# Performance work log

Measured on AMD Instinct MI355X. Metric: run time of the kernel, lower is better.

Reference implementation:

```python
import jax, jax.numpy as jnp
import numpy as np

N_HEAD = 16
N_EMBD = 1024
B, T = 4, 1024


def setup_inputs() -> dict:
    key = jax.random.key(0)
    ks = jax.random.split(key, 8)
    hs = N_EMBD // N_HEAD
    x = jax.random.normal(ks[0], (B, T, N_EMBD), dtype=jnp.float32)
    # previous-layer attention load per token, ~O(1/T) like a softmax column mean
    refractory_state = jax.random.uniform(ks[1], (B, T), dtype=jnp.float32) / T
    s_attn = 1.0 / np.sqrt(N_EMBD)
    W_attn = jax.random.normal(ks[2], (N_EMBD, 3 * N_EMBD), dtype=jnp.float32) * s_attn
    b_attn = jnp.zeros((3 * N_EMBD,), dtype=jnp.float32)
    W_proj = jax.random.normal(ks[3], (N_EMBD, N_EMBD), dtype=jnp.float32) * s_attn
    b_proj = jnp.zeros((N_EMBD,), dtype=jnp.float32)
    # learnable LIF params, init per module (lif_mode='refractory')
    threshold = jnp.full((N_HEAD,), 0.01, dtype=jnp.float32)
    leak = jnp.full((N_HEAD,), 2.0, dtype=jnp.float32)
    steepness = jnp.full((N_HEAD,), 2.0, dtype=jnp.float32)
    ref_strength = jnp.full((N_HEAD,), -2.0, dtype=jnp.float32)
    cross_w = jnp.full((N_HEAD,), -2.0, dtype=jnp.float32)
    return {
        "x": x, "refractory_state": refractory_state,
        "W_attn": W_attn, "b_attn": b_attn,
        "W_proj": W_proj, "b_proj": b_proj,
        "threshold": threshold, "leak": leak, "steepness": steepness,
        "ref_strength": ref_strength, "cross_w": cross_w,
    }


def reference(x, refractory_state, W_attn, b_attn, W_proj, b_proj,
              threshold, leak, steepness, ref_strength, cross_w):
    Bq, Tq, C = x.shape
    H = N_HEAD
    hs = C // H
    qkv = x @ W_attn + b_attn                     # [B,T,3C]
    q, k, v = jnp.split(qkv, 3, axis=-1)
    q = q.reshape(Bq, Tq, H, hs).transpose(0, 2, 1, 3)  # [B,H,T,hs]
    k = k.reshape(Bq, Tq, H, hs).transpose(0, 2, 1, 3)
    v = v.reshape(Bq, Tq, H, hs).transpose(0, 2, 1, 3)

    att = jnp.einsum('bhqd,bhkd->bhqk', q, k) * (1.0 / jnp.sqrt(jnp.asarray(hs, x.dtype)))
    causal = jnp.tril(jnp.ones((Tq, Tq), dtype=bool))
    att = jnp.where(causal[None, None], att, -jnp.inf)
    probs = jax.nn.softmax(att, axis=-1)          # [B,H,T,T]

    thr = (jnp.abs(threshold) * 0.1)[None, :, None, None]
    lk = jax.nn.sigmoid(leak)[None, :, None, None]
    st = jax.nn.softplus(steepness)[None, :, None, None]
    # refractory: column load over queries + cross-layer load
    column_load = probs.mean(axis=-2, keepdims=True)          # [B,H,1,T]
    eff_thr = thr + jax.nn.softplus(ref_strength)[None, :, None, None] * column_load
    eff_thr = eff_thr + jax.nn.sigmoid(cross_w)[None, :, None, None] * refractory_state[:, None, None, :]

    fire = jax.nn.sigmoid(st * (probs - eff_thr))
    lif_w = fire + lk * (1.0 - fire)
    mod = probs * lif_w
    mod = mod / (mod.sum(axis=-1, keepdims=True) + 1e-8)
    new_refractory = mod.mean(axis=1).mean(axis=-2)           # [B,T]

    y = jnp.einsum('bhqk,bhkd->bhqd', mod, v)
    y = y.transpose(0, 2, 1, 3).reshape(Bq, Tq, C)
    y = y @ W_proj + b_proj
    return y, new_refractory
```

## Files before the change

kernel.cpp:

```cpp
#include <hip/hip_runtime.h>
#include <math.h>

#define B_  4
#define T_  1024
#define C_  1024
#define H_  16
#define HS_ 64
#define K2E 0.1803368801f
#define LOG2E 1.44269504f

typedef _Float16 f16;
typedef _Float16 f16x8 __attribute__((ext_vector_type(8)));
typedef _Float16 f16x4 __attribute__((ext_vector_type(4)));
typedef float f32x4 __attribute__((ext_vector_type(4)));

#define MFMA16(a,b,c) __builtin_amdgcn_mfma_f32_16x16x32_f16(a,b,c,0,0,0)
#define EXP2(x) __builtin_amdgcn_exp2f(x)
#define RCP(x)  __builtin_amdgcn_rcpf(x)

#define PSTRIDE_BH 557056

__device__ __forceinline__ float qsum_(float v){
    v += __shfl_xor(v,1,64); v += __shfl_xor(v,2,64);
    v += __shfl_xor(v,4,64); v += __shfl_xor(v,8,64);
    return v;
}
__device__ __forceinline__ float sigmoidf_(float x){ return 1.0f/(1.0f + __expf(-x)); }
__device__ __forceinline__ float softplusf_(float x){ return fmaxf(x, 0.0f) + log1pf(__expf(-fabsf(x))); }

__device__ __forceinline__ void gload_lds16(const f16* g, f16* l){
    __builtin_amdgcn_global_load_lds(
        (__attribute__((address_space(1))) void*)(void*)g,
        (__attribute__((address_space(3))) void*)(void*)l, 16, 0, 0);
}

__global__ __launch_bounds__(256) void prep_k(
    const float* __restrict__ x, const float* __restrict__ Wa,
    const float* __restrict__ Wp,
    f16* __restrict__ x_h, f16* __restrict__ WaT, f16* __restrict__ WpT,
    float* __restrict__ zbase)
{
    __shared__ float tl[32][33];
    const int bid = blockIdx.x, tid = threadIdx.x;
    if (bid < 2048){
        int i = bid*256 + tid;
        const float4* p = (const float4*)x + (size_t)i*2;
        float4 a = p[0], b = p[1];
        f16x8 o;
        o[0]=(f16)a.x; o[1]=(f16)a.y; o[2]=(f16)a.z; o[3]=(f16)a.w;
        o[4]=(f16)b.x; o[5]=(f16)b.y; o[6]=(f16)b.z; o[7]=(f16)b.w;
        *((f16x8*)x_h + i) = o;
    } else if (bid < 5120){
        int t = bid - 2048;
        int n0 = (t % 96)*32, k0 = (t / 96)*32;
        const int c = tid & 31, r4 = tid >> 5;
        #pragma unroll
        for (int i=0;i<4;i++){ int r = r4*4+i; tl[r][c] = Wa[(size_t)(k0+r)*3072 + n0 + c]; }
        __syncthreads();
        #pragma unroll
        for (int i=0;i<4;i++){ int r = r4*4+i; WaT[(size_t)(n0+r)*1024 + k0 + c] = (f16)tl[c][r]; }
    } else if (bid < 6144){
        int t = bid - 5120;
        int n0 = (t & 31)*32, k0 = (t >> 5)*32;
        const int c = tid & 31, r4 = tid >> 5;
        #pragma unroll
        for (int i=0;i<4;i++){ int r = r4*4+i; tl[r][c] = Wp[(size_t)(k0+r)*1024 + n0 + c]; }
        __syncthreads();
        #pragma unroll
        for (int i=0;i<4;i++){ int r = r4*4+i; WpT[(size_t)(n0+r)*1024 + k0 + c] = (f16)tl[c][r]; }
    } else {
        int idx = (bid - 6144)*256 + tid;
        float4 z; z.x=0.f; z.y=0.f; z.z=0.f; z.w=0.f;
        ((float4*)zbase)[idx] = z;
    }
}

#define CT_STRIDE 132
__global__ __launch_bounds__(256) void gemm_qkv_k(
    const f16* __restrict__ A, const f16* __restrict__ Bt,
    const float* __restrict__ bias,
    f16* __restrict__ Qh, f16* __restrict__ Kh, f16* __restrict__ Vt)
{
    __shared__ __align__(16) f16 smem[16896];
    const int tid = threadIdx.x;
    const int lane = tid & 63, wave = tid >> 6;
    const int lx = lane & 15, quad = lane >> 4;
    const int wm = wave & 1, wn = wave >> 1;
    const int lin = blockIdx.y*24 + blockIdx.x;
    const int nb  = (lin & 7)*96 + (lin >> 3);
    const int m0 = (nb/24)*128, n0 = (nb%24)*128;
    const f16* Ap = A  + (size_t)m0*1024;
    const f16* Bp = Bt + (size_t)n0*1024;
    f32x4 acc[4][4];
    #pragma unroll
    for (int i=0;i<4;i++){
        #pragma unroll
        for (int j=0;j<4;j++){ acc[i][j][0]=0.f;acc[i][j][1]=0.f;acc[i][j][2]=0.f;acc[i][j][3]=0.f; }
    }
#define GQ_STAGE(BUF, KT) { \
    const int k0s = (KT)*32; \
    for (int i=0;i<2;i++){ int c=i*4+wave; \
        gload_lds16(Ap + (size_t)(c*16+lx)*1024 + k0s + quad*8, &smem[(BUF) + c*512]); \
        gload_lds16(Bp + (size_t)(c*16+lx)*1024 + k0s + quad*8, &smem[(BUF) + 4096 + c*512]); } }
#define GQ_COMP(BUF) { \
    f16x8 af[4], bf[4]; \
    for (int mt=0;mt<4;mt++) af[mt] = *(const f16x8*)&smem[(BUF) + (wm*4+mt)*512 + quad*128 + lx*8]; \
    for (int nt=0;nt<4;nt++) bf[nt] = *(const f16x8*)&smem[(BUF) + 4096 + (wn*4+nt)*512 + quad*128 + lx*8]; \
    for (int mt=0;mt<4;mt++) \
        for (int nt=0;nt<4;nt++) \
            acc[mt][nt] = MFMA16(af[mt], bf[nt], acc[mt][nt]); }

    GQ_STAGE(0, 0);
    __syncthreads();
    #pragma unroll 1
    for (int it=0; it<32; it+=2){
        if (it+1 < 32) GQ_STAGE(8192, it+1);
        GQ_COMP(0);
        __syncthreads();
        if (it+2 < 32) GQ_STAGE(0, it+2);
        GQ_COMP(8192);
        __syncthreads();
    }
    f16* Ct = smem;
    #pragma unroll
    for (int mt=0;mt<4;mt++){
        #pragma unroll
        for (int nt=0;nt<4;nt++){
            int n_loc = wn*64 + nt*16 + lx;
            float bv = bias[n0 + n_loc];
            #pragma unroll
            for (int r=0;r<4;r++){
                int m_loc = wm*64 + mt*16 + quad*4 + r;
                Ct[m_loc*CT_STRIDE + n_loc] = (f16)(acc[mt][nt][r] + bv);
            }
        }
    }
    __syncthreads();
    const int bb = m0 >> 10;
    if (n0 < 2048){
        for (int it=0; it<8; it++){
            int row = it*32 + wave*8 + (lane>>3);
            int ch  = lane & 7;
            int m_loc = row >> 1, half = row & 1;
            f16x8 v = *(const f16x8*)&Ct[m_loc*CT_STRIDE + half*64 + ch*8];
            int n = n0 + half*64;
            int which = n >> 10, cc = n & 1023, h = cc >> 6;
            int t = (m0 + m_loc) & 1023;
            f16* dst = (which==0) ? Qh : Kh;
            *(f16x8*)(dst + ((size_t)(bb*16+h)*1024 + t)*64 + ch*8) = v;
        }
    } else {
        for (int it=0; it<8; it++){
            int drow = it*16 + wave*4 + (lane>>4);
            int ch   = lane & 15;
            int cc = (n0 + drow) & 1023;
            int h = cc >> 6, d = cc & 63;
            f16 tmp[8];
            #pragma unroll
            for (int j=0;j<8;j++) tmp[j] = Ct[(ch*8+j)*CT_STRIDE + drow];
            int t = (m0 + ch*8) & 1023;
            *(f16x8*)(Vt + ((size_t)(bb*16+h)*64 + d)*1024 + t) = *(f16x8*)tmp;
        }
    }
}

__global__ __launch_bounds__(256) void gemm_proj_k(
    const f16* __restrict__ A, const f16* __restrict__ Bt,
    const float* __restrict__ bias, float* __restrict__ out,
    const float* __restrict__ racc)
{
    if (blockIdx.x == 512){
        float* oref = out + (size_t)B_*T_*C_;
        #pragma unroll
        for (int j=0;j<16;j++){
            int idx = j*256 + threadIdx.x;
            oref[idx] = racc[idx] * (1.0f/(H_*T_));
        }
        return;
    }
    __shared__ __align__(16) f16 smem[12288];
    const int tid = threadIdx.x;
    const int lane = tid & 63, wave = tid >> 6;
    const int lx = lane & 15, quad = lane >> 4;
    const int wm = wave & 1, wn = wave >> 1;
    const int lin = blockIdx.x;
    const int nb  = (lin & 7)*64 + (lin >> 3);
    const int m0 = (nb >> 4)*128, n0 = (nb & 15)*64;
    const f16* Ap = A  + (size_t)m0*1024;
    const f16* Bp = Bt + (size_t)n0*1024;
    f32x4 acc[4][2];
    #pragma unroll
    for (int i=0;i<4;i++){
        #pragma unroll
        for (int j=0;j<2;j++){ acc[i][j][0]=0.f;acc[i][j][1]=0.f;acc[i][j][2]=0.f;acc[i][j][3]=0.f; }
    }
#define GP_STAGE(BUF, KT) { \
    const int k0s = (KT)*32; \
    for (int i=0;i<2;i++){ int c=i*4+wave; \
        gload_lds16(Ap + (size_t)(c*16+lx)*1024 + k0s + quad*8, &smem[(BUF) + c*512]); } \
    gload_lds16(Bp + (size_t)(wave*16+lx)*1024 + k0s + quad*8, &smem[(BUF) + 4096 + wave*512]); }
#define GP_COMP(BUF) { \
    f16x8 af[4], bf[2]; \
    for (int mt=0;mt<4;mt++) af[mt] = *(const f16x8*)&smem[(BUF) + (wm*4+mt)*512 + quad*128 + lx*8]; \
    for (int nt=0;nt<2;nt++) bf[nt] = *(const f16x8*)&smem[(BUF) + 4096 + (wn*2+nt)*512 + quad*128 + lx*8]; \
    for (int mt=0;mt<4;mt++) \
        for (int nt=0;nt<2;nt++) \
            acc[mt][nt] = MFMA16(af[mt], bf[nt], acc[mt][nt]); }

    GP_STAGE(0, 0);
    __syncthreads();
    #pragma unroll 1
    for (int it=0; it<32; it+=2){
        if (it+1 < 32) GP_STAGE(6144, it+1);
        GP_COMP(0);
        __syncthreads();
        if (it+2 < 32) GP_STAGE(0, it+2);
        GP_COMP(6144);
        __syncthreads();
    }
    #pragma unroll
    for (int mt=0;mt<4;mt++){
        #pragma unroll
        for (int nt=0;nt<2;nt++){
            int n = n0 + wn*32 + nt*16 + lx;
            float bv = bias[n];
            #pragma unroll
            for (int r=0;r<4;r++){
                int m = m0 + wm*64 + mt*16 + quad*4 + r;
                out[(size_t)m*1024 + n] = acc[mt][nt][r] + bv;
            }
        }
    }
}

__global__ __launch_bounds__(256) void attn_stats_k(
    const f16* __restrict__ Qh, const f16* __restrict__ Kh,
    float* __restrict__ rowl, float* __restrict__ colp,
    f16* __restrict__ Pbuf)
{
    __shared__ __align__(16) f16 Pl[4][16*72];
    __shared__ float invl_sh[64];
    const int tid = threadIdx.x;
    const int lane = tid & 63, wave = tid >> 6;
    const int lx = lane & 15, quad = lane >> 4;
    const int g  = 15 - (blockIdx.x >> 6);
    const int bh = blockIdx.x & 63;
    const int qpos = wave*16 + quad*4;
    const size_t kbase = (size_t)bh*65536;
    const int S = (g+1)*64;
    f16* __restrict__ Pblk = Pbuf + (size_t)bh*PSTRIDE_BH + (size_t)4096*((g*(g+1))>>1);

    const size_t qoff = ((size_t)bh*1024 + g*64 + wave*16 + lx)*64;
    f16x8 aq0 = *(const f16x8*)(Qh + qoff + quad*8);
    f16x8 aq1 = *(const f16x8*)(Qh + qoff + 32 + quad*8);

#define KLOADX(dst, KT) { \
    for (int nt=0;nt<4;nt++){ \
        const f16* kp = Kh + kbase + (size_t)((KT)*64 + nt*16 + lx)*64 + quad*8; \
        dst[nt*2]   = *(const f16x8*)(kp); \
        dst[nt*2+1] = *(const f16x8*)(kp + 32); } }
#define STATS_TILE(KT, rk) { \
    const bool diag = ((KT) == g); \
    for (int nt=0;nt<4;nt++){ \
        f32x4 sc = {0.f,0.f,0.f,0.f}; \
        sc = MFMA16(aq0, rk[nt*2],   sc); \
        sc = MFMA16(aq1, rk[nt*2+1], sc); \
        for (int r=0;r<4;r++){ \
            float sv = sc[r]; \
            if (diag && (nt*16+lx) > (qpos + r)) sv = -1e4f; \
            float p = EXP2(sv*K2E); \
            ls[r] += p; \
            Pl[wave][(quad*4+r)*72 + nt*16 + lx] = (f16)p; \
        } } \
    for (int it2=0; it2<2; it2++){ \
        int qq = it2*8 + (lane>>3), chh = lane & 7; \
        f16x8 v = *(const f16x8*)&Pl[wave][qq*72 + chh*8]; \
        *(f16x8*)(Pblk + (size_t)(wave*16+qq)*S + (KT)*64 + chh*8) = v; } }

    f16x8 rkE[8], rkO[8];
    float ls[4] = {0.f,0.f,0.f,0.f};
    KLOADX(rkE, 0);
    if (g >= 1) KLOADX(rkO, 1);
    #pragma unroll 1
    for (int kt=0; kt<=g; kt+=2){
        STATS_TILE(kt, rkE);
        if (kt+2 <= g) KLOADX(rkE, kt+2);
        if (kt+1 <= g){
            STATS_TILE(kt+1, rkO);
            if (kt+3 <= g) KLOADX(rkO, kt+3);
        }
    }
    #pragma unroll
    for (int r=0;r<4;r++){
        float l = qsum_(ls[r]);
        if (lx == 0){
            rowl[(size_t)bh*1024 + g*64 + qpos + r] = l;
            invl_sh[qpos + r] = RCP(l);
        }
    }
    __syncthreads();
    if (tid < (g+1)*16){
        const int k0 = tid*4;
        float a0=0.f, a1=0.f, a2=0.f, a3=0.f;
        const f16* pr = Pblk + k0;
        #pragma unroll 4
        for (int q=0;q<64;q++){
            f16x4 v = *(const f16x4*)(pr + (size_t)q*S);
            float w = invl_sh[q];
            a0 += (float)v[0]*w; a1 += (float)v[1]*w;
            a2 += (float)v[2]*w; a3 += (float)v[3]*w;
        }
        float* cp = colp + (size_t)bh*1024 + k0;
        atomicAdd(cp+0,a0); atomicAdd(cp+1,a1);
        atomicAdd(cp+2,a2); atomicAdd(cp+3,a3);
    }
}

__global__ __launch_bounds__(256) void attn_apply_k(
    const f16* __restrict__ Vt,
    const float* __restrict__ rowl,
    const float* __restrict__ colp, const float* __restrict__ refr,
    const float* __restrict__ threshold, const float* __restrict__ leak,
    const float* __restrict__ steepness, const float* __restrict__ ref_strength,
    const float* __restrict__ cross_w,
    f16* __restrict__ Yh, float* __restrict__ racc,
    f16* __restrict__ Pbuf)
{
    __shared__ __align__(16) f16 Pl[4][16*72];
    __shared__ float eb[1024];
    __shared__ float invl_sh[64];
    __shared__ float invD_sh[64];
    const int tid = threadIdx.x;
    const int lane = tid & 63, wave = tid >> 6;
    const int lx = lane & 15, quad = lane >> 4;
    const int g  = 15 - (blockIdx.x >> 6);
    const int bh = blockIdx.x & 63;
    const int b  = bh >> 4, h = bh & 15;
    const size_t kbase = (size_t)bh*65536;
    const int S = (g+1)*64;
    f16* __restrict__ Pblk = Pbuf + (size_t)bh*PSTRIDE_BH + (size_t)4096*((g*(g+1))>>1);

    const float thr = fabsf(threshold[h])*0.1f;
    const float lk  = sigmoidf_(leak[h]);
    const float st2 = softplusf_(steepness[h]) * LOG2E;
    const float sprT= softplusf_(ref_strength[h]) * (1.0f/T_);
    const float cw  = sigmoidf_(cross_w[h]);
    const float Alk = 1.f - lk;

    {
        float4 cp = *(const float4*)(colp + (size_t)bh*1024 + tid*4);
        float4 rf = *(const float4*)(refr + (size_t)b*1024 + tid*4);
        eb[tid*4+0] = st2*(thr + sprT*cp.x + cw*rf.x);
        eb[tid*4+1] = st2*(thr + sprT*cp.y + cw*rf.y);
        eb[tid*4+2] = st2*(thr + sprT*cp.z + cw*rf.z);
        eb[tid*4+3] = st2*(thr + sprT*cp.w + cw*rf.w);
    }
    if (tid < 64) invl_sh[tid] = RCP(rowl[(size_t)bh*1024 + g*64 + tid]);
    __syncthreads();

    const float wli = invl_sh[wave*16 + lx];

    f32x4 y[4];
    #pragma unroll
    for (int i=0;i<4;i++){ y[i][0]=0.f;y[i][1]=0.f;y[i][2]=0.f;y[i][3]=0.f; }
    float Dp = 0.f;

#define PLOADX(dst, KT) { \
    const f16* pp = Pblk + (size_t)(wave*16 + lx)*S + (KT)*64 + quad*8; \
    dst[0] = *(const f16x8*)(pp); \
    dst[1] = *(const f16x8*)(pp + 32); }
#define RVLOAD(dst, KT) { \
    for (int dt=0;dt<4;dt++){ \
        const f16* vp = Vt + kbase + (size_t)(dt*16 + lx)*1024 + (KT)*64 + quad*8; \
        dst[dt*2]   = *(const f16x8*)(vp); \
        dst[dt*2+1] = *(const f16x8*)(vp + 32); } }
#define LIF_TILE(KT, pv, af0, af1) { \
    const float* ebp = &eb[(KT)*64 + quad*8]; \
    float4 eA0 = *(const float4*)(ebp); \
    float4 eA1 = *(const float4*)(ebp+4); \
    float4 eB0 = *(const float4*)(ebp+32); \
    float4 eB1 = *(const float4*)(ebp+36); \
    float ea[8] = {eA0.x,eA0.y,eA0.z,eA0.w,eA1.x,eA1.y,eA1.z,eA1.w}; \
    float ebb[8] = {eB0.x,eB0.y,eB0.z,eB0.w,eB1.x,eB1.y,eB1.z,eB1.w}; \
    for (int jj=0;jj<8;jj++){ \
        float p = (float)pv[0][jj] * wli; \
        float fire = RCP(1.f + EXP2(ea[jj] - st2*p)); \
        float pw = p*(lk + Alk*fire); \
        Dp += pw; af0[jj] = (f16)pw; } \
    for (int jj=0;jj<8;jj++){ \
        float p = (float)pv[1][jj] * wli; \
        float fire = RCP(1.f + EXP2(ebb[jj] - st2*p)); \
        float pw = p*(lk + Alk*fire); \
        Dp += pw; af1[jj] = (f16)pw; } }
#define MFMA8(af0, af1, rv) { \
    for (int dt=0;dt<4;dt++){ \
        y[dt] = MFMA16(af0, rv[dt*2],   y[dt]); \
        y[dt] = MFMA16(af1, rv[dt*2+1], y[dt]); } }

    f16x8 rv[8], pvE[2], pvO[2], af0, af1;
    PLOADX(pvE, 0);
    if (g >= 1) PLOADX(pvO, 1);
    #pragma unroll 1
    for (int kt=0; kt<=g; kt+=2){
        RVLOAD(rv, kt);
        LIF_TILE(kt, pvE, af0, af1);
        if (kt+2 <= g) PLOADX(pvE, kt+2);
        MFMA8(af0, af1, rv);
        if (kt+1 <= g){
            RVLOAD(rv, kt+1);
            LIF_TILE(kt+1, pvO, af0, af1);
            if (kt+3 <= g) PLOADX(pvO, kt+3);
            MFMA8(af0, af1, rv);
        }
    }
    Dp += __shfl_xor(Dp,16,64); Dp += __shfl_xor(Dp,32,64);
    float invDl = RCP(Dp + 1e-8f);
    if (quad == 0) invD_sh[wave*16 + lx] = invDl;

    float invD[4];
    #pragma unroll
    for (int r=0;r<4;r++) invD[r] = invD_sh[wave*16 + quad*4 + r];
    #pragma unroll
    for (int dt=0;dt<4;dt++){
        #pragma unroll
        for (int r=0;r<4;r++)
            Pl[wave][(quad*4+r)*72 + dt*16 + lx] = (f16)(y[dt][r]*invD[r]);
    }
    #pragma unroll
    for (int it=0; it<2; it++){
        int q = it*8 + (lane>>3), ch = lane & 7;
        f16x8 v = *(const f16x8*)&Pl[wave][q*72 + ch*8];
        *(f16x8*)(Yh + (size_t)(b*1024 + g*64 + wave*16 + q)*1024 + h*64 + ch*8) = v;
    }

    __syncthreads();

    if (tid < (g+1)*16){
        const int k0 = tid*4;
        float4 ebv = *(const float4*)&eb[k0];
        float a0=0.f, a1=0.f, a2=0.f, a3=0.f;
        const f16* pr = Pblk + k0;
        #pragma unroll 4
        for (int q=0;q<64;q++){
            f16x4 v = *(const f16x4*)(pr + (size_t)q*S);
            float wl = invl_sh[q], wd = invD_sh[q];
            float p0 = (float)v[0]*wl, p1 = (float)v[1]*wl;
            float p2 = (float)v[2]*wl, p3 = (float)v[3]*wl;
            float f0 = RCP(1.f + EXP2(ebv.x - st2*p0));
            float f1 = RCP(1.f + EXP2(ebv.y - st2*p1));
            float f2 = RCP(1.f + EXP2(ebv.z - st2*p2));
            float f3 = RCP(1.f + EXP2(ebv.w - st2*p3));
            a0 += p0*(lk + Alk*f0)*wd; a1 += p1*(lk + Alk*f1)*wd;
            a2 += p2*(lk + Alk*f2)*wd; a3 += p3*(lk + Alk*f3)*wd;
        }
        float* rp = racc + (size_t)b*1024 + k0;
        atomicAdd(rp+0,a0); atomicAdd(rp+1,a1);
        atomicAdd(rp+2,a2); atomicAdd(rp+3,a3);
    }
}

extern "C" void kernel_launch(void* const* d_in, const int* in_sizes, int n_in,
                              void* d_out, int out_size, void* d_ws, size_t ws_size,
                              hipStream_t stream) {
    (void)in_sizes; (void)n_in; (void)out_size; (void)ws_size;
    const float* x           = (const float*)d_in[0];
    const float* refr        = (const float*)d_in[1];
    const float* W_attn      = (const float*)d_in[2];
    const float* b_attn      = (const float*)d_in[3];
    const float* W_proj      = (const float*)d_in[4];
    const float* b_proj      = (const float*)d_in[5];
    const float* threshold   = (const float*)d_in[6];
    const float* leak        = (const float*)d_in[7];
    const float* steepness   = (const float*)d_in[8];
    const float* ref_strength= (const float*)d_in[9];
    const float* cross_w     = (const float*)d_in[10];
    float* out = (float*)d_out;

    char* ws = (char*)d_ws;
    f16* x_h = (f16*)ws;                       ws += (size_t)4096*1024*2;
    f16* WaT = (f16*)ws;                       ws += (size_t)3072*1024*2;
    f16* WpT = (f16*)ws;                       ws += (size_t)1024*1024*2;
    f16* Qh  = (f16*)ws;                       ws += (size_t)64*1024*64*2;
    f16* Kh  = (f16*)ws;                       ws += (size_t)64*1024*64*2;
    f16* Vt  = (f16*)ws;                       ws += (size_t)64*64*1024*2;
    f16* Yh  = (f16*)ws;                       ws += (size_t)4096*1024*2;
    float* rowl = (float*)ws;                  ws += (size_t)65536*4;
    float* colp = (float*)ws;                  ws += (size_t)65536*4;
    float* racc = (float*)ws;                  ws += (size_t)4096*4;
    f16* Pbuf = (f16*)ws;                      ws += (size_t)64*PSTRIDE_BH*2;

    prep_k<<<dim3(6212), dim3(256), 0, stream>>>(x, W_attn, W_proj, x_h, WaT, WpT, colp);
    gemm_qkv_k<<<dim3(24,32), dim3(256), 0, stream>>>(x_h, WaT, b_attn, Qh, Kh, Vt);
    attn_stats_k<<<dim3(1024), dim3(256), 0, stream>>>(Qh, Kh, rowl, colp, Pbuf);
    attn_apply_k<<<dim3(1024), dim3(256), 0, stream>>>(
        Vt, rowl, colp, refr,
        threshold, leak, steepness, ref_strength, cross_w, Yh, racc, Pbuf);
    gemm_proj_k<<<dim3(513), dim3(256), 0, stream>>>(Yh, WpT, b_proj, out, racc);
}
```

Measured before the change: 293.0 us.

## Stage K tiles through shared memory and double-buffer V loads in LIF pass

In the stats kernel, each wave now loads a quarter of each K tile into registers and writes it into a double-buffered LDS tile. All four waves then read the full tile from LDS, so the same K rows are no longer fetched from global memory by every wave. This cuts K register footprint from 16 to 4 vectors but adds block barriers per tile. In the LIF/PV kernel, V tiles are prefetched into two register sets one tile ahead, and MFMA blocks are raised in wave priority with s_setprio. This increases register pressure.

```diff
diff --git a/kernel.cpp b/kernel.cpp
--- a/kernel.cpp
+++ b/kernel.cpp
@@ -238,6 +238,7 @@
     float* __restrict__ rowl, float* __restrict__ colp,
     f16* __restrict__ Pbuf)
 {
+    __shared__ __align__(16) f16 Kl[8192];
     __shared__ __align__(16) f16 Pl[4][16*72];
     __shared__ float invl_sh[64];
     const int tid = threadIdx.x;
@@ -254,17 +255,20 @@
     f16x8 aq0 = *(const f16x8*)(Qh + qoff + quad*8);
     f16x8 aq1 = *(const f16x8*)(Qh + qoff + 32 + quad*8);
 
-#define KLOADX(dst, KT) { \
-    for (int nt=0;nt<4;nt++){ \
-        const f16* kp = Kh + kbase + (size_t)((KT)*64 + nt*16 + lx)*64 + quad*8; \
-        dst[nt*2]   = *(const f16x8*)(kp); \
-        dst[nt*2+1] = *(const f16x8*)(kp + 32); } }
-#define STATS_TILE(KT, rk) { \
+#define KLOAD(dst, KT) { \
+    for (int i=0;i<2;i++){ int u=i*4+wave, cc=u&3, kh=u>>2; \
+        dst[i] = *(const f16x8*)(Kh + kbase + (size_t)((KT)*64 + cc*16+lx)*64 + kh*32 + quad*8); } }
+#define KSTORE(src, BUF) { \
+    for (int i=0;i<2;i++){ int u=i*4+wave, cc=u&3, kh=u>>2; \
+        *(f16x8*)&Kl[(BUF) + cc*1024 + kh*512 + quad*128 + lx*8] = src[i]; } }
+#define STATS1_TILE(KT, BUF) { \
     const bool diag = ((KT) == g); \
     for (int nt=0;nt<4;nt++){ \
         f32x4 sc = {0.f,0.f,0.f,0.f}; \
-        sc = MFMA16(aq0, rk[nt*2],   sc); \
-        sc = MFMA16(aq1, rk[nt*2+1], sc); \
+        f16x8 b0 = *(const f16x8*)&Kl[(BUF) + nt*1024 + quad*128 + lx*8]; \
+        f16x8 b1 = *(const f16x8*)&Kl[(BUF) + nt*1024 + 512 + quad*128 + lx*8]; \
+        sc = MFMA16(aq0, b0, sc); \
+        sc = MFMA16(aq1, b1, sc); \
         for (int r=0;r<4;r++){ \
             float sv = sc[r]; \
             if (diag && (nt*16+lx) > (qpos + r)) sv = -1e4f; \
@@ -277,17 +281,23 @@
         f16x8 v = *(const f16x8*)&Pl[wave][qq*72 + chh*8]; \
         *(f16x8*)(Pblk + (size_t)(wave*16+qq)*S + (KT)*64 + chh*8) = v; } }
 
-    f16x8 rkE[8], rkO[8];
+    f16x8 rkE[2], rkO[2];
     float ls[4] = {0.f,0.f,0.f,0.f};
-    KLOADX(rkE, 0);
-    if (g >= 1) KLOADX(rkO, 1);
+    KLOAD(rkE, 0);
+    KSTORE(rkE, 0);
+    if (g >= 1) KLOAD(rkO, 1);
+    __syncthreads();
     #pragma unroll 1
     for (int kt=0; kt<=g; kt+=2){
-        STATS_TILE(kt, rkE);
-        if (kt+2 <= g) KLOADX(rkE, kt+2);
+        if (kt+2 <= g) KLOAD(rkE, kt+2);
+        if (kt+1 <= g) KSTORE(rkO, 4096);
+        STATS1_TILE(kt, 0);
+        __syncthreads();
         if (kt+1 <= g){
-            STATS_TILE(kt+1, rkO);
-            if (kt+3 <= g) KLOADX(rkO, kt+3);
+            if (kt+3 <= g) KLOAD(rkO, kt+3);
+            if (kt+2 <= g) KSTORE(rkE, 0);
+            STATS1_TILE(kt+1, 4096);
+            __syncthreads();
         }
     }
     #pragma unroll
@@ -393,24 +403,26 @@
         float pw = p*(lk + Alk*fire); \
         Dp += pw; af1[jj] = (f16)pw; } }
 #define MFMA8(af0, af1, rv) { \
+    __builtin_amdgcn_s_setprio(1); \
     for (int dt=0;dt<4;dt++){ \
         y[dt] = MFMA16(af0, rv[dt*2],   y[dt]); \
-        y[dt] = MFMA16(af1, rv[dt*2+1], y[dt]); } }
-
-    f16x8 rv[8], pvE[2], pvO[2], af0, af1;
-    PLOADX(pvE, 0);
-    if (g >= 1) PLOADX(pvO, 1);
+        y[dt] = MFMA16(af1, rv[dt*2+1], y[dt]); } \
+    __builtin_amdgcn_s_setprio(0); }
+
+    f16x8 rvA[8], rvB[8], pvA[2], pvB[2], af0, af1;
+    PLOADX(pvA, 0); RVLOAD(rvA, 0);
+    if (g >= 1){ PLOADX(pvB, 1); RVLOAD(rvB, 1); }
     #pragma unroll 1
     for (int kt=0; kt<=g; kt+=2){
-        RVLOAD(rv, kt);
-        LIF_TILE(kt, pvE, af0, af1);
-        if (kt+2 <= g) PLOADX(pvE, kt+2);
-        MFMA8(af0, af1, rv);
+        LIF_TILE(kt, pvA, af0, af1);
+        if (kt+2 <= g) PLOADX(pvA, kt+2);
+        MFMA8(af0, af1, rvA);
+        if (kt+2 <= g) RVLOAD(rvA, kt+2);
         if (kt+1 <= g){
-            RVLOAD(rv, kt+1);
-            LIF_TILE(kt+1, pvO, af0, af1);
-            if (kt+3 <= g) PLOADX(pvO, kt+3);
-            MFMA8(af0, af1, rv);
+            LIF_TILE(kt+1, pvB, af0, af1);
+            if (kt+3 <= g) PLOADX(pvB, kt+3);
+            MFMA8(af0, af1, rvB);
+            if (kt+3 <= g) RVLOAD(rvB, kt+3);
         }
     }
     Dp += __shfl_xor(Dp,16,64); Dp += __shfl_xor(Dp,32,64);
```

Result: faster. 277.0 us (-5.5%).
